# Kernel optimization log

Hardware: AMD Instinct MI355X
Metric: run time of the kernel (lower is better)

## Reference

```python
import jax, jax.numpy as jnp
import numpy as np

NEG_INF = -1e30

def setup_inputs() -> dict:
    key = jax.random.key(0)
    ks = jax.random.split(key, 7)
    B, S, D = 2, 4096, 128
    scale = 1.0 / np.sqrt(D)
    return {
        "x": jax.random.normal(ks[0], (B, S, D), jnp.float32),
        "Wq": jax.random.normal(ks[1], (D, D), jnp.float32) * scale,
        "bq": jax.random.normal(ks[2], (D,), jnp.float32) * 0.01,
        "Wk": jax.random.normal(ks[3], (D, D), jnp.float32) * scale,
        "bk": jax.random.normal(ks[4], (D,), jnp.float32) * 0.01,
        "Wv": jax.random.normal(ks[5], (D, D), jnp.float32) * scale,
        "bv": jax.random.normal(ks[6], (D,), jnp.float32) * 0.01,
        "window_size": 128,
    }

def reference(x, Wq, bq, Wk, bk, Wv, bv, window_size):
    B, S, D = x.shape
    half = window_size // 2
    q = x @ Wq + bq
    k = x @ Wk + bk
    v = x @ Wv + bv
    # banded window indices: for query i, keys in [i-half, i+half]
    offs = jnp.arange(-half, half + 1)          # [W] with W = 2*half+1
    idx = jnp.arange(S)[:, None] + offs[None, :]  # [S, W]
    valid = (idx >= 0) & (idx < S)
    idxc = jnp.clip(idx, 0, S - 1)
    kw = k[:, idxc, :]  # [B, S, W, D]
    vw = v[:, idxc, :]  # [B, S, W, D]
    scores = jnp.einsum('bsd,bswd->bsw', q, kw) / jnp.sqrt(jnp.float32(D))
    scores = jnp.where(valid[None], scores, NEG_INF)
    attn = jax.nn.softmax(scores, axis=-1)
    out = jnp.einsum('bsw,bswd->bsd', attn, vw)
    return out
```

## Files before the change

### kernel.cpp

```cpp
#include <hip/hip_runtime.h>
#include <hip/hip_bf16.h>

typedef __attribute__((ext_vector_type(8))) short short8;
typedef __attribute__((ext_vector_type(4))) float f32x4;

union U16x8 { uint4 u; short8 s; unsigned short us[8]; };

#define S_LEN 4096
#define DH    128
#define TQ    16
#define VTS   168
#define PST   168
#define XSTR  136

__global__ __launch_bounds__(256) void qkv_kernel(
    const float* __restrict__ x,
    const float* __restrict__ Wq, const float* __restrict__ bq,
    const float* __restrict__ Wk, const float* __restrict__ bk,
    const float* __restrict__ Wv, const float* __restrict__ bv,
    __hip_bfloat16* __restrict__ q, __hip_bfloat16* __restrict__ k,
    __hip_bfloat16* __restrict__ v)
{
    __shared__ __align__(16) unsigned short XH[32 * XSTR];
    __shared__ __align__(16) unsigned short XL[32 * XSTR];

    const int t = threadIdx.x;
    const int row0 = blockIdx.x * 32;
    const int mat = blockIdx.y;

    #pragma unroll
    for (int p = 0; p < 4; ++p) {
        int c = t + p * 256;
        int r = c >> 5, cg = c & 31;
        float4 xv = *(const float4*)(x + (size_t)(row0 + r) * DH + cg * 4);
        unsigned h[2], l[2];
        #pragma unroll
        for (int hw = 0; hw < 2; ++hw) {
            unsigned hh[2], ll[2];
            #pragma unroll
            for (int j = 0; j < 2; ++j) {
                float xs = (&xv.x)[hw * 2 + j];
                __hip_bfloat16 hb = __float2bfloat16(xs);
                float hf = __bfloat162float(hb);
                __hip_bfloat16 lb = __float2bfloat16(xs - hf);
                hh[j] = *(unsigned short*)&hb;
                ll[j] = *(unsigned short*)&lb;
            }
            h[hw] = hh[0] | (hh[1] << 16);
            l[hw] = ll[0] | (ll[1] << 16);
        }
        *(uint2*)&XH[r * XSTR + cg * 4] = make_uint2(h[0], h[1]);
        *(uint2*)&XL[r * XSTR + cg * 4] = make_uint2(l[0], l[1]);
    }
    __syncthreads();

    const int wave = t >> 6, lane = t & 63;
    const int i = lane & 15, g = lane >> 4;

    short8 ah[2][4], al[2][4];
    #pragma unroll
    for (int rt = 0; rt < 2; ++rt)
        #pragma unroll
        for (int kc = 0; kc < 4; ++kc) {
            ah[rt][kc] = *(const short8*)&XH[(rt*16 + i) * XSTR + kc*32 + g*8];
            al[rt][kc] = *(const short8*)&XL[(rt*16 + i) * XSTR + kc*32 + g*8];
        }

    const float* W = (mat == 0) ? Wq : (mat == 1) ? Wk : Wv;
    const float* bias_p = (mat == 0) ? bq : (mat == 1) ? bk : bv;
    __hip_bfloat16* O = (mat == 0) ? q : (mat == 1) ? k : v;

    #pragma unroll
    for (int ct = 0; ct < 2; ++ct) {
        const int col = wave*32 + ct*16 + i;
        const float bias = bias_p[col];

        short8 bf[4];
        #pragma unroll
        for (int kc = 0; kc < 4; ++kc) {
            const float* wp = W + (size_t)(kc*32 + g*8) * DH + col;
            U16x8 u;
            #pragma unroll
            for (int j = 0; j < 8; ++j) {
                __hip_bfloat16 wb = __float2bfloat16(wp[(size_t)j * DH]);
                u.us[j] = *(unsigned short*)&wb;
            }
            bf[kc] = u.s;
        }

        #pragma unroll
        for (int rt = 0; rt < 2; ++rt) {
            f32x4 acc; acc[0]=0.f; acc[1]=0.f; acc[2]=0.f; acc[3]=0.f;
            #pragma unroll
            for (int kc = 0; kc < 4; ++kc) {
                acc = __builtin_amdgcn_mfma_f32_16x16x32_bf16(ah[rt][kc], bf[kc], acc, 0, 0, 0);
                acc = __builtin_amdgcn_mfma_f32_16x16x32_bf16(al[rt][kc], bf[kc], acc, 0, 0, 0);
            }
            #pragma unroll
            for (int r = 0; r < 4; ++r) {
                O[(size_t)(row0 + rt*16 + g*4 + r) * DH + col] =
                    __float2bfloat16(acc[r] + bias);
            }
        }
    }
}

__device__ inline void vt_xpose_write(unsigned short* VT, const uint4* vr,
                                      int kgp, int dgp)
{
    unsigned w[8][4];
    #pragma unroll
    for (int p = 0; p < 4; ++p) {
        #pragma unroll
        for (int j = 0; j < 4; ++j) {
            unsigned xlo = ((const unsigned*)&vr[2*p])[j];
            unsigned ylo = ((const unsigned*)&vr[2*p+1])[j];
            w[2*j][p]   = __builtin_amdgcn_perm(ylo, xlo, 0x05040100u);
            w[2*j+1][p] = __builtin_amdgcn_perm(ylo, xlo, 0x07060302u);
        }
    }
    int sw = kgp + (dgp & 7); if (sw >= 21) sw -= 21;
    #pragma unroll
    for (int d = 0; d < 8; ++d) {
        int row = dgp*8 + d;
        *(uint4*)&VT[row*VTS + sw*8] =
            make_uint4(w[d][0], w[d][1], w[d][2], w[d][3]);
    }
}

__global__ __launch_bounds__(256) void attn_kernel(
    const __hip_bfloat16* __restrict__ qg,
    const __hip_bfloat16* __restrict__ kg,
    const __hip_bfloat16* __restrict__ vg,
    float* __restrict__ out, const int* __restrict__ wsz)
{
    __shared__ __align__(16) unsigned short VT[128 * VTS];
    __shared__ __align__(16) unsigned short Pm[TQ * PST];
    __shared__ float pmax[4][16];
    __shared__ float psum[4][16];

    const int t    = threadIdx.x;
    const int wave = t >> 6, lane = t & 63;
    const int i = lane & 15, g = lane >> 4;
    const int bid  = blockIdx.x;
    const int qblk = (bid & 7) * 64 + (bid >> 3);
    const int b    = qblk >> 8;
    const int s0   = (qblk & 255) * TQ;
    const int k0   = s0 - 64;
    const int half = wsz[0] >> 1;
    const float scale = 0.08838834764831845f;

    const __hip_bfloat16* kb = kg + (size_t)b * S_LEN * DH;
    const __hip_bfloat16* vb = vg + (size_t)b * S_LEN * DH;

    const int kgp0 = t >> 4, dgp0 = t & 15;
    const bool two = (t & 3) == 0;
    const int tau2 = 256 + (t >> 2);
    const int kgp1 = tau2 >> 4, dgp1 = tau2 & 15;
    uint4 vr0[8], vr1[8];
    #pragma unroll
    for (int r = 0; r < 8; ++r) {
        int key = k0 + kgp0*8 + r;
        uint4 val = make_uint4(0u,0u,0u,0u);
        if (key >= 0 && key < S_LEN)
            val = *(const uint4*)(vb + (size_t)key * DH + dgp0*8);
        vr0[r] = val;
    }
    #pragma unroll
    for (int r = 0; r < 8; ++r) {
        int key = k0 + kgp1*8 + r;
        uint4 val = make_uint4(0u,0u,0u,0u);
        if (two && key >= 0 && key < S_LEN)
            val = *(const uint4*)(vb + (size_t)key * DH + dgp1*8);
        vr1[r] = val;
    }

    short8 aq[4];
    {
        const __hip_bfloat16* qrow = qg + (size_t)(b * S_LEN + s0 + i) * DH;
        #pragma unroll
        for (int kc = 0; kc < 4; ++kc) {
            U16x8 u; u.u = *(const uint4*)(qrow + kc*32 + g*8);
            aq[kc] = u.s;
        }
    }

    const int nkt = (wave < 2) ? 3 : 2;
    f32x4 acc[3];
    #pragma unroll
    for (int u = 0; u < 3; ++u) { acc[u][0]=0.f; acc[u][1]=0.f; acc[u][2]=0.f; acc[u][3]=0.f; }
    #pragma unroll
    for (int u = 0; u < 3; ++u) {
        if (u < nkt) {
            int kt = wave + 4*u;
            int key = k0 + kt*16 + i;
            const __hip_bfloat16* krow = kb + (ptrdiff_t)key * DH;
            #pragma unroll
            for (int kc = 0; kc < 4; ++kc) {
                U16x8 u16v; u16v.u = *(const uint4*)(krow + kc*32 + g*8);
                acc[u] = __builtin_amdgcn_mfma_f32_16x16x32_bf16(aq[kc], u16v.s, acc[u], 0, 0, 0);
            }
        }
    }

    vt_xpose_write(VT, vr0, kgp0, dgp0);
    if (two) vt_xpose_write(VT, vr1, kgp1, dgp1);

    float sc[3][4], m4[4];
    #pragma unroll
    for (int r = 0; r < 4; ++r) m4[r] = -3e30f;
    #pragma unroll
    for (int u = 0; u < 3; ++u) {
        if (u < nkt) {
            int kt = wave + 4*u;
            int key = k0 + kt*16 + i;
            #pragma unroll
            for (int r = 0; r < 4; ++r) {
                int qrow = s0 + g*4 + r;
                bool valid = (key >= 0) && (key < S_LEN) &&
                             (key >= qrow - half) && (key <= qrow + half);
                float sv = valid ? acc[u][r] * scale : -1e30f;
                sc[u][r] = sv;
                m4[r] = fmaxf(m4[r], sv);
            }
        }
    }
    #pragma unroll
    for (int r = 0; r < 4; ++r) {
        #pragma unroll
        for (int m = 1; m < 16; m <<= 1)
            m4[r] = fmaxf(m4[r], __shfl_xor(m4[r], m, 64));
    }
    if (i == 0) {
        #pragma unroll
        for (int r = 0; r < 4; ++r) pmax[wave][g*4 + r] = m4[r];
    }
    __syncthreads();

    float M[4], l4[4];
    #pragma unroll
    for (int r = 0; r < 4; ++r) {
        int qr = g*4 + r;
        M[r] = fmaxf(fmaxf(pmax[0][qr], pmax[1][qr]), fmaxf(pmax[2][qr], pmax[3][qr]));
        l4[r] = 0.f;
    }
    #pragma unroll
    for (int u = 0; u < 3; ++u) {
        if (u < nkt) {
            int kt = wave + 4*u;
            #pragma unroll
            for (int r = 0; r < 4; ++r) {
                float p = __expf(sc[u][r] - M[r]);
                l4[r] += p;
                __hip_bfloat16 pb = __float2bfloat16(p);
                Pm[(g*4 + r) * PST + kt*16 + i] = *(unsigned short*)&pb;
            }
        }
    }
    #pragma unroll
    for (int r = 0; r < 4; ++r) {
        #pragma unroll
        for (int m = 1; m < 16; m <<= 1)
            l4[r] += __shfl_xor(l4[r], m, 64);
    }
    if (i == 0) {
        #pragma unroll
        for (int r = 0; r < 4; ++r) psum[wave][g*4 + r] = l4[r];
    }
    __syncthreads();

    float linv[4];
    #pragma unroll
    for (int r = 0; r < 4; ++r) {
        int qr = g*4 + r;
        linv[r] = 1.0f / (psum[0][qr] + psum[1][qr] + psum[2][qr] + psum[3][qr]);
    }

    short8 ap[5];
    #pragma unroll
    for (int kc = 0; kc < 5; ++kc)
        ap[kc] = *(const short8*)&Pm[i * PST + kc*32 + g*8];

    const int n0 = wave * 32;
    f32x4 oacc[2];
    #pragma unroll
    for (int nt = 0; nt < 2; ++nt) { oacc[nt][0]=0.f; oacc[nt][1]=0.f; oacc[nt][2]=0.f; oacc[nt][3]=0.f; }
    #pragma unroll
    for (int nt = 0; nt < 2; ++nt) {
        int row0 = n0 + nt*16 + i;
        int dgr = (row0 >> 3) & 7;
        #pragma unroll
        for (int kc = 0; kc < 5; ++kc) {
            int lg = 4*kc + g;
            int sw = lg + dgr; if (sw >= 21) sw -= 21;
            short8 bv = *(const short8*)&VT[row0 * VTS + sw*8];
            oacc[nt] = __builtin_amdgcn_mfma_f32_16x16x32_bf16(ap[kc], bv, oacc[nt], 0, 0, 0);
        }
    }

    #pragma unroll
    for (int nt = 0; nt < 2; ++nt) {
        #pragma unroll
        for (int r = 0; r < 4; ++r) {
            int qrow = s0 + g*4 + r;
            out[((size_t)(b * S_LEN) + qrow) * DH + n0 + nt*16 + i] = oacc[nt][r] * linv[r];
        }
    }
}

extern "C" void kernel_launch(void* const* d_in, const int* in_sizes, int n_in,
                              void* d_out, int out_size, void* d_ws, size_t ws_size,
                              hipStream_t stream) {
    const float* x  = (const float*)d_in[0];
    const float* Wq = (const float*)d_in[1];
    const float* bq = (const float*)d_in[2];
    const float* Wk = (const float*)d_in[3];
    const float* bk = (const float*)d_in[4];
    const float* Wv = (const float*)d_in[5];
    const float* bv = (const float*)d_in[6];
    const int* wsz  = (const int*)d_in[7];

    const int B = 2, S = 4096;
    const int N = B * S;

    __hip_bfloat16* q = (__hip_bfloat16*)d_ws;
    __hip_bfloat16* k = q + (size_t)N * DH;
    __hip_bfloat16* v = k + (size_t)N * DH;

    qkv_kernel<<<dim3(256, 3), 256, 0, stream>>>(x, Wq, bq, Wk, bk, Wv, bv, q, k, v);
    attn_kernel<<<N / TQ, 256, 0, stream>>>(q, k, v, (float*)d_out, wsz);
}
```

Measured before the change: 84.55 us.

## Fuse QKV projection and banded attention into one persistent kernel with grid barriers

Merges the QKV projection and attention kernels into a single 512-block kernel that uses software grid-wide barriers. Each block first converts its own 16 rows of x to split bf16 and a slice of the weights to transposed bf16, then computes Q/K/V for its rows after a barrier, then runs attention after a second barrier. This removes a kernel launch and the strided fp32 weight gathers, at the cost of two grid syncs. It relies on all 512 blocks being co-resident (launch_bounds 256,2), otherwise it can deadlock.

```diff
diff --git a/kernel.cpp b/kernel.cpp
--- a/kernel.cpp
+++ b/kernel.cpp
@@ -12,97 +12,27 @@
 #define VTS   168
 #define PST   168
 #define XSTR  136
-
-__global__ __launch_bounds__(256) void qkv_kernel(
-    const float* __restrict__ x,
-    const float* __restrict__ Wq, const float* __restrict__ bq,
-    const float* __restrict__ Wk, const float* __restrict__ bk,
-    const float* __restrict__ Wv, const float* __restrict__ bv,
-    __hip_bfloat16* __restrict__ q, __hip_bfloat16* __restrict__ k,
-    __hip_bfloat16* __restrict__ v)
-{
-    __shared__ __align__(16) unsigned short XH[32 * XSTR];
-    __shared__ __align__(16) unsigned short XL[32 * XSTR];
-
-    const int t = threadIdx.x;
-    const int row0 = blockIdx.x * 32;
-    const int mat = blockIdx.y;
-
-    #pragma unroll
-    for (int p = 0; p < 4; ++p) {
-        int c = t + p * 256;
-        int r = c >> 5, cg = c & 31;
-        float4 xv = *(const float4*)(x + (size_t)(row0 + r) * DH + cg * 4);
-        unsigned h[2], l[2];
-        #pragma unroll
-        for (int hw = 0; hw < 2; ++hw) {
-            unsigned hh[2], ll[2];
-            #pragma unroll
-            for (int j = 0; j < 2; ++j) {
-                float xs = (&xv.x)[hw * 2 + j];
-                __hip_bfloat16 hb = __float2bfloat16(xs);
-                float hf = __bfloat162float(hb);
-                __hip_bfloat16 lb = __float2bfloat16(xs - hf);
-                hh[j] = *(unsigned short*)&hb;
-                ll[j] = *(unsigned short*)&lb;
-            }
-            h[hw] = hh[0] | (hh[1] << 16);
-            l[hw] = ll[0] | (ll[1] << 16);
-        }
-        *(uint2*)&XH[r * XSTR + cg * 4] = make_uint2(h[0], h[1]);
-        *(uint2*)&XL[r * XSTR + cg * 4] = make_uint2(l[0], l[1]);
-    }
-    __syncthreads();
-
-    const int wave = t >> 6, lane = t & 63;
-    const int i = lane & 15, g = lane >> 4;
-
-    short8 ah[2][4], al[2][4];
-    #pragma unroll
-    for (int rt = 0; rt < 2; ++rt)
-        #pragma unroll
-        for (int kc = 0; kc < 4; ++kc) {
-            ah[rt][kc] = *(const short8*)&XH[(rt*16 + i) * XSTR + kc*32 + g*8];
-            al[rt][kc] = *(const short8*)&XL[(rt*16 + i) * XSTR + kc*32 + g*8];
-        }
-
-    const float* W = (mat == 0) ? Wq : (mat == 1) ? Wk : Wv;
-    const float* bias_p = (mat == 0) ? bq : (mat == 1) ? bk : bv;
-    __hip_bfloat16* O = (mat == 0) ? q : (mat == 1) ? k : v;
-
-    #pragma unroll
-    for (int ct = 0; ct < 2; ++ct) {
-        const int col = wave*32 + ct*16 + i;
-        const float bias = bias_p[col];
-
-        short8 bf[4];
-        #pragma unroll
-        for (int kc = 0; kc < 4; ++kc) {
-            const float* wp = W + (size_t)(kc*32 + g*8) * DH + col;
-            U16x8 u;
-            #pragma unroll
-            for (int j = 0; j < 8; ++j) {
-                __hip_bfloat16 wb = __float2bfloat16(wp[(size_t)j * DH]);
-                u.us[j] = *(unsigned short*)&wb;
-            }
-            bf[kc] = u.s;
-        }
-
-        #pragma unroll
-        for (int rt = 0; rt < 2; ++rt) {
-            f32x4 acc; acc[0]=0.f; acc[1]=0.f; acc[2]=0.f; acc[3]=0.f;
-            #pragma unroll
-            for (int kc = 0; kc < 4; ++kc) {
-                acc = __builtin_amdgcn_mfma_f32_16x16x32_bf16(ah[rt][kc], bf[kc], acc, 0, 0, 0);
-                acc = __builtin_amdgcn_mfma_f32_16x16x32_bf16(al[rt][kc], bf[kc], acc, 0, 0, 0);
-            }
-            #pragma unroll
-            for (int r = 0; r < 4; ++r) {
-                O[(size_t)(row0 + rt*16 + g*4 + r) * DH + col] =
-                    __float2bfloat16(acc[r] + bias);
-            }
-        }
-    }
+#define NBLK  512
+
+__device__ unsigned g_cnt = 0;
+__device__ unsigned g_gen = 0;
+
+__device__ __forceinline__ void grid_barrier() {
+    __syncthreads();
+    __threadfence();
+    if (threadIdx.x == 0) {
+        unsigned gen = __hip_atomic_load(&g_gen, __ATOMIC_ACQUIRE, __HIP_MEMORY_SCOPE_AGENT);
+        unsigned old = __hip_atomic_fetch_add(&g_cnt, 1u, __ATOMIC_ACQ_REL, __HIP_MEMORY_SCOPE_AGENT);
+        if (old == NBLK - 1) {
+            __hip_atomic_store(&g_cnt, 0u, __ATOMIC_RELAXED, __HIP_MEMORY_SCOPE_AGENT);
+            __hip_atomic_fetch_add(&g_gen, 1u, __ATOMIC_ACQ_REL, __HIP_MEMORY_SCOPE_AGENT);
+        } else {
+            while (__hip_atomic_load(&g_gen, __ATOMIC_ACQUIRE, __HIP_MEMORY_SCOPE_AGENT) == gen)
+                __builtin_amdgcn_s_sleep(16);
+        }
+    }
+    __syncthreads();
+    __threadfence();
 }
 
 __device__ inline void vt_xpose_write(unsigned short* VT, const uint4* vr,
@@ -128,10 +58,13 @@
     }
 }
 
-__global__ __launch_bounds__(256) void attn_kernel(
-    const __hip_bfloat16* __restrict__ qg,
-    const __hip_bfloat16* __restrict__ kg,
-    const __hip_bfloat16* __restrict__ vg,
+__global__ __launch_bounds__(256, 2) void fused_kernel(
+    const float* __restrict__ x,
+    const float* __restrict__ Wq, const float* __restrict__ bq,
+    const float* __restrict__ Wk, const float* __restrict__ bk,
+    const float* __restrict__ Wv, const float* __restrict__ bv,
+    __hip_bfloat16* __restrict__ qg, __hip_bfloat16* __restrict__ kg,
+    __hip_bfloat16* __restrict__ vg, unsigned short* __restrict__ WT,
     float* __restrict__ out, const int* __restrict__ wsz)
 {
     __shared__ __align__(16) unsigned short VT[128 * VTS];
@@ -146,6 +79,78 @@
     const int qblk = (bid & 7) * 64 + (bid >> 3);
     const int b    = qblk >> 8;
     const int s0   = (qblk & 255) * TQ;
+    const int grow0 = b * S_LEN + s0;
+
+    unsigned short* XH = VT;
+    unsigned short* XL = VT + 16 * XSTR;
+
+    {
+        int r = t >> 4, cg = t & 15;
+        const float* xp = x + (size_t)(grow0 + r) * DH + cg * 8;
+        float4 va = *(const float4*)xp;
+        float4 vb = *(const float4*)(xp + 4);
+        float xs[8] = {va.x, va.y, va.z, va.w, vb.x, vb.y, vb.z, vb.w};
+        U16x8 h, l;
+        #pragma unroll
+        for (int j = 0; j < 8; ++j) {
+            __hip_bfloat16 hb = __float2bfloat16(xs[j]);
+            float hf = __bfloat162float(hb);
+            __hip_bfloat16 lb = __float2bfloat16(xs[j] - hf);
+            h.us[j] = *(unsigned short*)&hb;
+            l.us[j] = *(unsigned short*)&lb;
+        }
+        *(uint4*)&XH[r * XSTR + cg * 8] = h.u;
+        *(uint4*)&XL[r * XSTR + cg * 8] = l.u;
+    }
+
+    if (t < 96) {
+        int e = bid * 96 + t;
+        int mat = e >> 14, rem = e & 16383;
+        int kk = rem >> 7, col = rem & 127;
+        const float* W = (mat == 0) ? Wq : (mat == 1) ? Wk : Wv;
+        __hip_bfloat16 wb = __float2bfloat16(W[rem]);
+        WT[mat * 16384 + col * 128 + kk] = *(unsigned short*)&wb;
+    }
+    __syncthreads();
+
+    short8 ah[4], al[4];
+    #pragma unroll
+    for (int kc = 0; kc < 4; ++kc) {
+        ah[kc] = *(const short8*)&XH[i * XSTR + kc*32 + g*8];
+        al[kc] = *(const short8*)&XL[i * XSTR + kc*32 + g*8];
+    }
+
+    grid_barrier();
+
+    #pragma unroll
+    for (int jj = 0; jj < 6; ++jj) {
+        int job = wave * 6 + jj;
+        int mat = job >> 3, ct = job & 7;
+        const float* bias_p = (mat == 0) ? bq : (mat == 1) ? bk : bv;
+        __hip_bfloat16* O = (mat == 0) ? qg : (mat == 1) ? kg : vg;
+        int col = ct * 16 + i;
+        float bias = bias_p[col];
+        const unsigned short* wt = WT + mat * 16384 + col * 128;
+
+        short8 bf[4];
+        #pragma unroll
+        for (int kc = 0; kc < 4; ++kc)
+            bf[kc] = *(const short8*)(wt + kc*32 + g*8);
+
+        f32x4 acc; acc[0]=0.f; acc[1]=0.f; acc[2]=0.f; acc[3]=0.f;
+        #pragma unroll
+        for (int kc = 0; kc < 4; ++kc) {
+            acc = __builtin_amdgcn_mfma_f32_16x16x32_bf16(ah[kc], bf[kc], acc, 0, 0, 0);
+            acc = __builtin_amdgcn_mfma_f32_16x16x32_bf16(al[kc], bf[kc], acc, 0, 0, 0);
+        }
+        #pragma unroll
+        for (int r = 0; r < 4; ++r) {
+            O[(size_t)(grow0 + g*4 + r) * DH + col] = __float2bfloat16(acc[r] + bias);
+        }
+    }
+
+    grid_barrier();
+
     const int k0   = s0 - 64;
     const int half = wsz[0] >> 1;
     const float scale = 0.08838834764831845f;
@@ -177,7 +182,7 @@
 
     short8 aq[4];
     {
-        const __hip_bfloat16* qrow = qg + (size_t)(b * S_LEN + s0 + i) * DH;
+        const __hip_bfloat16* qrow = qg + (size_t)(grow0 + i) * DH;
         #pragma unroll
         for (int kc = 0; kc < 4; ++kc) {
             U16x8 u; u.u = *(const uint4*)(qrow + kc*32 + g*8);
@@ -326,7 +331,8 @@
     __hip_bfloat16* q = (__hip_bfloat16*)d_ws;
     __hip_bfloat16* k = q + (size_t)N * DH;
     __hip_bfloat16* v = k + (size_t)N * DH;
-
-    qkv_kernel<<<dim3(256, 3), 256, 0, stream>>>(x, Wq, bq, Wk, bk, Wv, bv, q, k, v);
-    attn_kernel<<<N / TQ, 256, 0, stream>>>(q, k, v, (float*)d_out, wsz);
+    unsigned short* WT = (unsigned short*)(v + (size_t)N * DH);
+
+    fused_kernel<<<NBLK, 256, 0, stream>>>(x, Wq, bq, Wk, bk, Wv, bv,
+                                           q, k, v, WT, (float*)d_out, wsz);
 }
```

Measured after the change: 324.6 us. 284% more time.

## Process 32 queries per attention block to share the V tile

Applied to the files above, without the earlier changes.

Doubles the query tile per attention block from 16 to 32 rows and uses 512 threads (8 waves), with two groups of four waves each handling 16 queries. The transposed V window in shared memory is loaded once per block and shared by both query groups, which cuts redundant V loads and transposes. In exchange the grid has half as many blocks, each larger, which may reduce occupancy and load balance. K tiles are still loaded separately per wave group.

```diff
diff --git a/kernel.cpp b/kernel.cpp
--- a/kernel.cpp
+++ b/kernel.cpp
@@ -8,7 +8,7 @@
 
 #define S_LEN 4096
 #define DH    128
-#define TQ    16
+#define TQ    32
 #define VTS   168
 #define PST   168
 #define XSTR  136
@@ -128,7 +128,7 @@
     }
 }
 
-__global__ __launch_bounds__(256) void attn_kernel(
+__global__ __launch_bounds__(512) void attn_kernel(
     const __hip_bfloat16* __restrict__ qg,
     const __hip_bfloat16* __restrict__ kg,
     const __hip_bfloat16* __restrict__ vg,
@@ -136,16 +136,17 @@
 {
     __shared__ __align__(16) unsigned short VT[128 * VTS];
     __shared__ __align__(16) unsigned short Pm[TQ * PST];
-    __shared__ float pmax[4][16];
-    __shared__ float psum[4][16];
+    __shared__ float pmax[8][16];
+    __shared__ float psum[8][16];
 
     const int t    = threadIdx.x;
     const int wave = t >> 6, lane = t & 63;
     const int i = lane & 15, g = lane >> 4;
+    const int qt = wave >> 2, wq = wave & 3;
     const int bid  = blockIdx.x;
-    const int qblk = (bid & 7) * 64 + (bid >> 3);
-    const int b    = qblk >> 8;
-    const int s0   = (qblk & 255) * TQ;
+    const int qblk = (bid & 7) * 32 + (bid >> 3);
+    const int b    = qblk >> 7;
+    const int s0   = (qblk & 127) * TQ;
     const int k0   = s0 - 64;
     const int half = wsz[0] >> 1;
     const float scale = 0.08838834764831845f;
@@ -154,30 +155,22 @@
     const __hip_bfloat16* vb = vg + (size_t)b * S_LEN * DH;
 
     const int kgp0 = t >> 4, dgp0 = t & 15;
-    const bool two = (t & 3) == 0;
-    const int tau2 = 256 + (t >> 2);
-    const int kgp1 = tau2 >> 4, dgp1 = tau2 & 15;
-    uint4 vr0[8], vr1[8];
-    #pragma unroll
-    for (int r = 0; r < 8; ++r) {
-        int key = k0 + kgp0*8 + r;
-        uint4 val = make_uint4(0u,0u,0u,0u);
-        if (key >= 0 && key < S_LEN)
-            val = *(const uint4*)(vb + (size_t)key * DH + dgp0*8);
-        vr0[r] = val;
-    }
-    #pragma unroll
-    for (int r = 0; r < 8; ++r) {
-        int key = k0 + kgp1*8 + r;
-        uint4 val = make_uint4(0u,0u,0u,0u);
-        if (two && key >= 0 && key < S_LEN)
-            val = *(const uint4*)(vb + (size_t)key * DH + dgp1*8);
-        vr1[r] = val;
+    const bool havev = (t < 320);
+    uint4 vr0[8];
+    if (havev) {
+        #pragma unroll
+        for (int r = 0; r < 8; ++r) {
+            int key = k0 + kgp0*8 + r;
+            uint4 val = make_uint4(0u,0u,0u,0u);
+            if (key >= 0 && key < S_LEN)
+                val = *(const uint4*)(vb + (size_t)key * DH + dgp0*8);
+            vr0[r] = val;
+        }
     }
 
     short8 aq[4];
     {
-        const __hip_bfloat16* qrow = qg + (size_t)(b * S_LEN + s0 + i) * DH;
+        const __hip_bfloat16* qrow = qg + (size_t)(b * S_LEN + s0 + qt*16 + i) * DH;
         #pragma unroll
         for (int kc = 0; kc < 4; ++kc) {
             U16x8 u; u.u = *(const uint4*)(qrow + kc*32 + g*8);
@@ -185,14 +178,14 @@
         }
     }
 
-    const int nkt = (wave < 2) ? 3 : 2;
+    const int nkt = (wq < 2) ? 3 : 2;
     f32x4 acc[3];
     #pragma unroll
     for (int u = 0; u < 3; ++u) { acc[u][0]=0.f; acc[u][1]=0.f; acc[u][2]=0.f; acc[u][3]=0.f; }
     #pragma unroll
     for (int u = 0; u < 3; ++u) {
         if (u < nkt) {
-            int kt = wave + 4*u;
+            int kt = wq + 4*u;
             int key = k0 + kt*16 + i;
             const __hip_bfloat16* krow = kb + (ptrdiff_t)key * DH;
             #pragma unroll
@@ -203,8 +196,7 @@
         }
     }
 
-    vt_xpose_write(VT, vr0, kgp0, dgp0);
-    if (two) vt_xpose_write(VT, vr1, kgp1, dgp1);
+    if (havev) vt_xpose_write(VT, vr0, kgp0, dgp0);
 
     float sc[3][4], m4[4];
     #pragma unroll
@@ -212,11 +204,11 @@
     #pragma unroll
     for (int u = 0; u < 3; ++u) {
         if (u < nkt) {
-            int kt = wave + 4*u;
+            int kt = wq + 4*u;
             int key = k0 + kt*16 + i;
             #pragma unroll
             for (int r = 0; r < 4; ++r) {
-                int qrow = s0 + g*4 + r;
+                int qrow = s0 + qt*16 + g*4 + r;
                 bool valid = (key >= 0) && (key < S_LEN) &&
                              (key >= qrow - half) && (key <= qrow + half);
                 float sv = valid ? acc[u][r] * scale : -1e30f;
@@ -241,19 +233,20 @@
     #pragma unroll
     for (int r = 0; r < 4; ++r) {
         int qr = g*4 + r;
-        M[r] = fmaxf(fmaxf(pmax[0][qr], pmax[1][qr]), fmaxf(pmax[2][qr], pmax[3][qr]));
+        M[r] = fmaxf(fmaxf(pmax[qt*4+0][qr], pmax[qt*4+1][qr]),
+                     fmaxf(pmax[qt*4+2][qr], pmax[qt*4+3][qr]));
         l4[r] = 0.f;
     }
     #pragma unroll
     for (int u = 0; u < 3; ++u) {
         if (u < nkt) {
-            int kt = wave + 4*u;
+            int kt = wq + 4*u;
             #pragma unroll
             for (int r = 0; r < 4; ++r) {
                 float p = __expf(sc[u][r] - M[r]);
                 l4[r] += p;
                 __hip_bfloat16 pb = __float2bfloat16(p);
-                Pm[(g*4 + r) * PST + kt*16 + i] = *(unsigned short*)&pb;
+                Pm[(qt*16 + g*4 + r) * PST + kt*16 + i] = *(unsigned short*)&pb;
             }
         }
     }
@@ -273,15 +266,16 @@
     #pragma unroll
     for (int r = 0; r < 4; ++r) {
         int qr = g*4 + r;
-        linv[r] = 1.0f / (psum[0][qr] + psum[1][qr] + psum[2][qr] + psum[3][qr]);
+        linv[r] = 1.0f / (psum[qt*4+0][qr] + psum[qt*4+1][qr] +
+                          psum[qt*4+2][qr] + psum[qt*4+3][qr]);
     }
 
     short8 ap[5];
     #pragma unroll
     for (int kc = 0; kc < 5; ++kc)
-        ap[kc] = *(const short8*)&Pm[i * PST + kc*32 + g*8];
-
-    const int n0 = wave * 32;
+        ap[kc] = *(const short8*)&Pm[(qt*16 + i) * PST + kc*32 + g*8];
+
+    const int n0 = wq * 32;
     f32x4 oacc[2];
     #pragma unroll
     for (int nt = 0; nt < 2; ++nt) { oacc[nt][0]=0.f; oacc[nt][1]=0.f; oacc[nt][2]=0.f; oacc[nt][3]=0.f; }
@@ -302,7 +296,7 @@
     for (int nt = 0; nt < 2; ++nt) {
         #pragma unroll
         for (int r = 0; r < 4; ++r) {
-            int qrow = s0 + g*4 + r;
+            int qrow = s0 + qt*16 + g*4 + r;
             out[((size_t)(b * S_LEN) + qrow) * DH + n0 + nt*16 + i] = oacc[nt][r] * linv[r];
         }
     }
@@ -328,5 +322,5 @@
     __hip_bfloat16* v = k + (size_t)N * DH;
 
     qkv_kernel<<<dim3(256, 3), 256, 0, stream>>>(x, Wq, bq, Wk, bk, Wv, bv, q, k, v);
-    attn_kernel<<<N / TQ, 256, 0, stream>>>(q, k, v, (float*)d_out, wsz);
+    attn_kernel<<<N / TQ, 512, 0, stream>>>(q, k, v, (float*)d_out, wsz);
 }
```

Result: no change. 83.92 us (-0.7%).
